# Optimization experiments

Measured on AMD Instinct MI355X. Metric: run time of the kernel, lower is better.

Reference implementation:

```python
import jax, jax.numpy as jnp
import numpy as np

V, E, H = 50000, 100, 128
B, S = 16, 4096
NUM_LEVELS = int(np.log2(S)) + 1  # 13; level l has S >> l nodes
# gate order in the 5-gate stack: i, f_l, f_r, o, u
XMAP = jnp.array([0, 1, 1, 2, 3])


def setup_inputs() -> dict:
    key = jax.random.key(0)
    ks = jax.random.split(key, 9)
    sE = 1.0 / np.sqrt(E)
    sH = 1.0 / np.sqrt(H)
    return {
        "embedding": jax.random.normal(ks[0], (V, E), jnp.float32) * 0.1,
        "W_x": jax.random.normal(ks[1], (4, H, E), jnp.float32) * sE,   # (i,f,o,u) x-projections
        "b_x": jax.random.normal(ks[2], (4, H), jnp.float32) * sE,
        "U_l": jax.random.normal(ks[3], (5, H, H), jnp.float32) * sH,   # (u_i_l,u_f_ll,u_f_rr,u_o_l,u_u_l) applied to h_left
        "b_l": jax.random.normal(ks[4], (5, H), jnp.float32) * sH,
        "U_r": jax.random.normal(ks[5], (5, H, H), jnp.float32) * sH,   # (u_i_r,u_f_lr,u_f_rl,u_o_r,u_u_r) applied to h_right
        "b_r": jax.random.normal(ks[6], (5, H), jnp.float32) * sH,
        "input_seq": jax.random.randint(ks[7], (B, S), 0, V, jnp.int32),
        "dep_tags": jax.random.randint(ks[8], (NUM_LEVELS - 1, S // 2), 0, S, jnp.int32),
    }


def _level_step(x5, h_l, h_r, c_l, c_r, U_l, b_l, U_r, b_r):
    # x5: [B,N,5,H] per-gate x contributions (w_*(x) incl. bias)
    pre = (x5
           + jnp.einsum('bnk,ghk->bngh', h_l, U_l) + b_l
           + jnp.einsum('bnk,ghk->bngh', h_r, U_r) + b_r)  # [B,N,5,H]
    i   = jax.nn.sigmoid(pre[:, :, 0])
    f_l = jax.nn.sigmoid(pre[:, :, 1])
    f_r = jax.nn.sigmoid(pre[:, :, 2])
    o   = jax.nn.sigmoid(pre[:, :, 3])
    u   = jnp.tanh(pre[:, :, 4])
    c = i * u + f_l * c_l + f_r * c_r
    h = o * jnp.tanh(c)
    return h, c


def reference(embedding, W_x, b_x, U_l, b_l, U_r, b_r, input_seq, dep_tags):
    b, s = input_seq.shape
    emb = embedding[input_seq]  # [B,S,E]
    xg = jnp.einsum('bse,ghe->bsgh', emb, W_x) + b_x  # [B,S,4,H]

    # level 0: every leaf is a token, children are zero
    z = jnp.zeros((b, s, xg.shape[-1]), xg.dtype)
    h, c = _level_step(xg[:, :, XMAP, :], z, z, z, z, U_l, b_l, U_r, b_r)

    for l in range(1, NUM_LEVELS):
        n = s >> l
        dep = dep_tags[l - 1, :n]                # token position re-embedded at each internal node
        x5 = xg[:, dep][:, :, XMAP, :]           # [B,N,5,H]
        hp = h.reshape(b, n, 2, -1)              # node i's children are (2i, 2i+1)
        cp = c.reshape(b, n, 2, -1)
        h, c = _level_step(x5, hp[:, :, 0], hp[:, :, 1], cp[:, :, 0], cp[:, :, 1],
                           U_l, b_l, U_r, b_r)
    return h[:, 0], c[:, 0]  # root (h, c): [B,H] each
```

## Files before the change

kernel.cpp:

```cpp
#include <hip/hip_runtime.h>
#include <hip/hip_bf16.h>

#define V_ 50000
#define E_ 100
#define H_ 128
#define B_ 16
#define S_ 4096

typedef unsigned short u16;
typedef unsigned int   u32;
typedef short bf16x8 __attribute__((ext_vector_type(8)));
typedef float f32x4  __attribute__((ext_vector_type(4)));

__device__ __forceinline__ float bf2f(u16 x) {
  return __uint_as_float(((u32)x) << 16);
}
__device__ __forceinline__ u16 f2bf(float x) {
  __hip_bfloat16 b = __float2bfloat16(x);
  return *reinterpret_cast<u16*>(&b);
}
__device__ __forceinline__ float sigm(float x) { return 1.0f / (1.0f + __expf(-x)); }
__device__ __forceinline__ float tanh_f(float x) {
  float e = __expf(2.0f * x);
  return 1.0f - 2.0f / (e + 1.0f);
}

#define PREP_N0 (V_ * 128)
#define PREP_N1 65536
#define PREP_N2 163840
#define PREP_N3 640
__global__ __launch_bounds__(256) void prep_all(
    const float* __restrict__ emb, const float* __restrict__ Wx,
    const float* __restrict__ Ul, const float* __restrict__ Ur,
    const float* __restrict__ bl, const float* __restrict__ br,
    const float* __restrict__ bx,
    u16* __restrict__ embB, u16* __restrict__ Bx, u16* __restrict__ Bu,
    float* __restrict__ bxs, float* __restrict__ bd)
{
  int i = blockIdx.x * 256 + threadIdx.x;
  if (i < PREP_N0) {
    int k = i & 127, t = i >> 7;
    embB[i] = (k < E_) ? f2bf(emb[t * E_ + k]) : (u16)0;
    return;
  }
  i -= PREP_N0;
  if (i < PREP_N1) {
    int j = i & 7, l = (i >> 3) & 63, s = (i >> 9) & 3, t = i >> 11;
    int k = s * 32 + (l >> 4) * 8 + j;
    int o = t * 16 + (l & 15);
    Bx[i] = (k < E_) ? f2bf(Wx[o * E_ + k]) : (u16)0;
    return;
  }
  i -= PREP_N1;
  if (i < PREP_N2) {
    int j = i & 7, l = (i >> 3) & 63, s = (i >> 9) & 7, t = i >> 12;
    int k = s * 32 + (l >> 4) * 8 + j;
    int gh = t * 16 + (l & 15);
    float v = (k < 128) ? Ul[gh * 128 + k] : Ur[gh * 128 + (k - 128)];
    Bu[i] = f2bf(v);
    return;
  }
  i -= PREP_N2;
  if (i < 512) {
    int g = i >> 7, hh = i & 127;
    int lg = (g == 0) ? 0 : (g == 1) ? 1 : (g == 2) ? 3 : 4;
    bxs[i] = bx[i] + bl[lg * 128 + hh] + br[lg * 128 + hh];
    return;
  }
  i -= 512;
  if (i < 128) bd[i] = (bl[256 + i] + br[256 + i]) - (bl[128 + i] + br[128 + i]);
}

#define XLDS 514
__global__ __launch_bounds__(512) void xg_mfma(
    const u16* __restrict__ embB, const u16* __restrict__ Bx,
    const float* __restrict__ bxs, const int* __restrict__ seq,
    ushort4* __restrict__ xg, u16* __restrict__ h0)
{
  __shared__ u16 lds[32 * XLDS];
  const int w = threadIdx.x >> 6, lane = threadIdx.x & 63;
  const int quad = lane >> 4, l15 = lane & 15;
  const int m0 = blockIdx.x * 32;

  f32x4 acc[2][4];
  #pragma unroll
  for (int r = 0; r < 2; ++r)
    #pragma unroll
    for (int t = 0; t < 4; ++t) acc[r][t] = (f32x4){0.f, 0.f, 0.f, 0.f};

  int tok0 = seq[m0 + l15];
  int tok1 = seq[m0 + 16 + l15];
  const u16* a0p = embB + (size_t)tok0 * 128 + quad * 8;
  const u16* a1p = embB + (size_t)tok1 * 128 + quad * 8;

  #pragma unroll
  for (int s = 0; s < 4; ++s) {
    bf16x8 a0 = *reinterpret_cast<const bf16x8*>(a0p + s * 32);
    bf16x8 a1 = *reinterpret_cast<const bf16x8*>(a1p + s * 32);
    #pragma unroll
    for (int ti = 0; ti < 4; ++ti) {
      int t = w * 4 + ti;
      bf16x8 b = *reinterpret_cast<const bf16x8*>(Bx + ((size_t)(t * 4 + s) * 64 + lane) * 8);
      acc[0][ti] = __builtin_amdgcn_mfma_f32_16x16x32_bf16(a0, b, acc[0][ti], 0, 0, 0);
      acc[1][ti] = __builtin_amdgcn_mfma_f32_16x16x32_bf16(a1, b, acc[1][ti], 0, 0, 0);
    }
  }

  const int g = w >> 1;
  #pragma unroll
  for (int ti = 0; ti < 4; ++ti) {
    int o = (w * 4 + ti) * 16 + l15;
    float bxo = bxs[o];
    int hhw = (w & 1) * 64 + ti * 16 + l15;
    #pragma unroll
    for (int r = 0; r < 2; ++r)
      #pragma unroll
      for (int reg = 0; reg < 4; ++reg) {
        int mrow = r * 16 + quad * 4 + reg;
        lds[mrow * XLDS + hhw * 4 + g] = f2bf(acc[r][ti][reg] + bxo);
      }
  }
  __syncthreads();

  #pragma unroll
  for (int i = 0; i < 8; ++i) {
    int pidx = i * 512 + threadIdx.x;
    int m = pidx >> 7, hh = pidx & 127;
    ushort4 v = *reinterpret_cast<const ushort4*>(&lds[m * XLDS + hh * 4]);
    size_t gm = (size_t)(m0 + m);
    xg[gm * 128 + hh] = v;
    float c = sigm(bf2f(v.x)) * tanh_f(bf2f(v.w));
    float h = sigm(bf2f(v.z)) * tanh_f(c);
    h0[gm * 128 + hh] = f2bf(h);
  }
}

template<bool REC>
__global__ __launch_bounds__(512) void level_mfma64(
    const ushort4* __restrict__ xg4, const int* __restrict__ deprow,
    const u16* __restrict__ Bu, const float* __restrict__ bd,
    const u16* __restrict__ hPrev, const float* __restrict__ cPrev,
    u16* __restrict__ hOut, float* __restrict__ cOut, int n, int ln2n)
{
  const int w = threadIdx.x >> 6, lane = threadIdx.x & 63;
  const int quad = lane >> 4, l15 = lane & 15;
  const int hh = w * 16 + l15;
  const int m0 = blockIdx.x * 64;

  ushort4 xv[16];
  #pragma unroll
  for (int i = 0; i < 16; ++i) {
    int m = m0 + (i >> 2) * 16 + quad * 4 + (i & 3);
    int j = m & (n - 1);
    int b = m >> ln2n;
    xv[i] = xg4[((size_t)b * S_ + deprow[j]) * 128 + hh];
  }

  f32x4 acc[4][5];
  #pragma unroll
  for (int r = 0; r < 4; ++r)
    #pragma unroll
    for (int g = 0; g < 5; ++g) acc[r][g] = (f32x4){0.f, 0.f, 0.f, 0.f};

  const u16* ap = hPrev + (size_t)(m0 + l15) * 256 + quad * 8;

  #pragma unroll
  for (int s = 0; s < 8; ++s) {
    bf16x8 a[4];
    #pragma unroll
    for (int r = 0; r < 4; ++r)
      a[r] = *reinterpret_cast<const bf16x8*>(ap + (size_t)r * 16 * 256 + s * 32);
    #pragma unroll
    for (int g = 0; g < 5; ++g) {
      int t = g * 8 + w;
      bf16x8 b = *reinterpret_cast<const bf16x8*>(Bu + ((size_t)(t * 8 + s) * 64 + lane) * 8);
      #pragma unroll
      for (int r = 0; r < 4; ++r)
        acc[r][g] = __builtin_amdgcn_mfma_f32_16x16x32_bf16(a[r], b, acc[r][g], 0, 0, 0);
    }
  }

  float bdv = bd[hh];
  #pragma unroll
  for (int i = 0; i < 16; ++i) {
    int r = i >> 2, reg = i & 3;
    int m = m0 + r * 16 + quad * 4 + reg;
    ushort4 v = xv[i];
    float x0 = bf2f(v.x), x1 = bf2f(v.y), x2 = bf2f(v.z), x3 = bf2f(v.w);
    float cl, cr;
    if constexpr (REC) {
      ushort4 vl = xg4[(size_t)(2 * m) * 128 + hh];
      ushort4 vr = xg4[(size_t)(2 * m + 1) * 128 + hh];
      cl = sigm(bf2f(vl.x)) * tanh_f(bf2f(vl.w));
      cr = sigm(bf2f(vr.x)) * tanh_f(bf2f(vr.w));
    } else {
      cl = cPrev[(size_t)m * 256 + hh];
      cr = cPrev[(size_t)m * 256 + 128 + hh];
    }
    float pi  = acc[r][0][reg] + x0;
    float pfl = acc[r][1][reg] + x1;
    float pfr = acc[r][2][reg] + x1 + bdv;
    float po  = acc[r][3][reg] + x2;
    float pu  = acc[r][4][reg] + x3;
    float c = sigm(pi) * tanh_f(pu) + sigm(pfl) * cl + sigm(pfr) * cr;
    float h = sigm(po) * tanh_f(c);
    hOut[(size_t)m * 128 + hh] = f2bf(h);
    cOut[(size_t)m * 128 + hh] = c;
  }
}

__global__ __launch_bounds__(512) void level_mfma(
    const ushort4* __restrict__ xg4, const int* __restrict__ deprow,
    const u16* __restrict__ Bu, const float* __restrict__ bd,
    const u16* __restrict__ hPrev, const float* __restrict__ cPrev,
    u16* __restrict__ hOut, float* __restrict__ cOut, int n, int ln2n)
{
  const int w = threadIdx.x >> 6, lane = threadIdx.x & 63;
  const int quad = lane >> 4, l15 = lane & 15;
  const int hh = w * 16 + l15;
  const int m0 = blockIdx.x * 32;

  ushort4 xv[8];
  float clv[8], crv[8];
  #pragma unroll
  for (int i = 0; i < 8; ++i) {
    int m = m0 + (i >> 2) * 16 + quad * 4 + (i & 3);
    int j = m & (n - 1);
    int b = m >> ln2n;
    int dj = deprow[j];
    xv[i] = xg4[((size_t)b * S_ + dj) * 128 + hh];
    clv[i] = cPrev[(size_t)m * 256 + hh];
    crv[i] = cPrev[(size_t)m * 256 + 128 + hh];
  }

  f32x4 acc[2][5];
  #pragma unroll
  for (int r = 0; r < 2; ++r)
    #pragma unroll
    for (int g = 0; g < 5; ++g) acc[r][g] = (f32x4){0.f, 0.f, 0.f, 0.f};

  const u16* a0p = hPrev + (size_t)(m0 + l15) * 256 + quad * 8;
  const u16* a1p = a0p + 16 * 256;

  #pragma unroll
  for (int s = 0; s < 8; ++s) {
    bf16x8 a0 = *reinterpret_cast<const bf16x8*>(a0p + s * 32);
    bf16x8 a1 = *reinterpret_cast<const bf16x8*>(a1p + s * 32);
    #pragma unroll
    for (int g = 0; g < 5; ++g) {
      int t = g * 8 + w;
      bf16x8 b = *reinterpret_cast<const bf16x8*>(Bu + ((size_t)(t * 8 + s) * 64 + lane) * 8);
      acc[0][g] = __builtin_amdgcn_mfma_f32_16x16x32_bf16(a0, b, acc[0][g], 0, 0, 0);
      acc[1][g] = __builtin_amdgcn_mfma_f32_16x16x32_bf16(a1, b, acc[1][g], 0, 0, 0);
    }
  }

  float bdv = bd[hh];
  #pragma unroll
  for (int i = 0; i < 8; ++i) {
    int r = i >> 2, reg = i & 3;
    int m = m0 + r * 16 + quad * 4 + reg;
    ushort4 v = xv[i];
    float x0 = bf2f(v.x), x1 = bf2f(v.y), x2 = bf2f(v.z), x3 = bf2f(v.w);
    float pi  = acc[r][0][reg] + x0;
    float pfl = acc[r][1][reg] + x1;
    float pfr = acc[r][2][reg] + x1 + bdv;
    float po  = acc[r][3][reg] + x2;
    float pu  = acc[r][4][reg] + x3;
    float c = sigm(pi) * tanh_f(pu) + sigm(pfl) * clv[i] + sigm(pfr) * crv[i];
    float h = sigm(po) * tanh_f(c);
    hOut[(size_t)m * 128 + hh] = f2bf(h);
    cOut[(size_t)m * 128 + hh] = c;
  }
}

__global__ __launch_bounds__(512) void deep_fused(
    const ushort4* __restrict__ xg4, const int* __restrict__ dep,
    const u16* __restrict__ Bu, const float* __restrict__ bd,
    const u16* __restrict__ h6, const float* __restrict__ c6,
    float* __restrict__ out)
{
  __shared__ u16  hls[2][32 * 136];
  __shared__ float cls[2][32 * 128];
  const int b = blockIdx.x;
  const int w = threadIdx.x >> 6, lane = threadIdx.x & 63;
  const int quad = lane >> 4, l15 = lane & 15;
  const int hh = w * 16 + l15;

  const float bdv = bd[hh];

  {
    ushort4 xv[2][4];
    float clv[2][4], crv[2][4];
    #pragma unroll
    for (int r = 0; r < 2; ++r)
      #pragma unroll
      for (int reg = 0; reg < 4; ++reg) {
        int j = r * 16 + quad * 4 + reg;
        int dj = dep[6 * 2048 + j];
        xv[r][reg] = xg4[((size_t)b * S_ + dj) * 128 + hh];
        clv[r][reg] = c6[(size_t)(b * 32 + j) * 256 + hh];
        crv[r][reg] = c6[(size_t)(b * 32 + j) * 256 + 128 + hh];
      }

    f32x4 acc[2][5];
    #pragma unroll
    for (int r = 0; r < 2; ++r)
      #pragma unroll
      for (int g = 0; g < 5; ++g) acc[r][g] = (f32x4){0.f, 0.f, 0.f, 0.f};

    #pragma unroll
    for (int s = 0; s < 8; ++s) {
      const u16* ap = h6 + (size_t)(b * 32 + l15) * 256 + s * 32 + quad * 8;
      bf16x8 a0 = *reinterpret_cast<const bf16x8*>(ap);
      bf16x8 a1 = *reinterpret_cast<const bf16x8*>(ap + 16 * 256);
      #pragma unroll
      for (int g = 0; g < 5; ++g) {
        int t = g * 8 + w;
        bf16x8 bb = *reinterpret_cast<const bf16x8*>(Bu + ((size_t)(t * 8 + s) * 64 + lane) * 8);
        acc[0][g] = __builtin_amdgcn_mfma_f32_16x16x32_bf16(a0, bb, acc[0][g], 0, 0, 0);
        acc[1][g] = __builtin_amdgcn_mfma_f32_16x16x32_bf16(a1, bb, acc[1][g], 0, 0, 0);
      }
    }

    #pragma unroll
    for (int r = 0; r < 2; ++r)
      #pragma unroll
      for (int reg = 0; reg < 4; ++reg) {
        int j = r * 16 + quad * 4 + reg;
        ushort4 v = xv[r][reg];
        float x0 = bf2f(v.x), x1 = bf2f(v.y), x2 = bf2f(v.z), x3 = bf2f(v.w);
        float pi  = acc[r][0][reg] + x0;
        float pfl = acc[r][1][reg] + x1;
        float pfr = acc[r][2][reg] + x1 + bdv;
        float po  = acc[r][3][reg] + x2;
        float pu  = acc[r][4][reg] + x3;
        float c = sigm(pi) * tanh_f(pu) + sigm(pfl) * clv[r][reg] + sigm(pfr) * crv[r][reg];
        float h = sigm(po) * tanh_f(c);
        hls[0][j * 136 + hh] = f2bf(h);
        cls[0][j * 128 + hh] = c;
      }
  }
  __syncthreads();

  ushort4 xvc[4];
  #pragma unroll
  for (int reg = 0; reg < 4; ++reg)
    xvc[reg] = xg4[((size_t)b * S_ + dep[7 * 2048 + quad * 4 + reg]) * 128 + hh];

  int pb = 0;
  for (int lvl = 8; lvl <= 12; ++lvl) {
    int nb = 4096 >> lvl;

    ushort4 xvn[4];
    if (lvl < 12) {
      int nbn = 2048 >> lvl;
      #pragma unroll
      for (int reg = 0; reg < 4; ++reg) {
        int j = quad * 4 + reg;
        if (j < nbn)
          xvn[reg] = xg4[((size_t)b * S_ + dep[lvl * 2048 + j]) * 128 + hh];
      }
    }

    f32x4 acc[5];
    #pragma unroll
    for (int g = 0; g < 5; ++g) acc[g] = (f32x4){0.f, 0.f, 0.f, 0.f};

    #pragma unroll
    for (int s = 0; s < 8; ++s) {
      int child = 2 * l15 + (s >= 4 ? 1 : 0);
      int kk = (s & 3) * 32 + quad * 8;
      bf16x8 a = *reinterpret_cast<const bf16x8*>(&hls[pb][child * 136 + kk]);
      #pragma unroll
      for (int g = 0; g < 5; ++g) {
        int t = g * 8 + w;
        bf16x8 bb = *reinterpret_cast<const bf16x8*>(Bu + ((size_t)(t * 8 + s) * 64 + lane) * 8);
        acc[g] = __builtin_amdgcn_mfma_f32_16x16x32_bf16(a, bb, acc[g], 0, 0, 0);
      }
    }

    #pragma unroll
    for (int reg = 0; reg < 4; ++reg) {
      int j = quad * 4 + reg;
      if (j < nb) {
        ushort4 v = xvc[reg];
        float x0 = bf2f(v.x), x1 = bf2f(v.y), x2 = bf2f(v.z), x3 = bf2f(v.w);
        float cl = cls[pb][(2 * j) * 128 + hh];
        float cr = cls[pb][(2 * j + 1) * 128 + hh];
        float pi  = acc[0][reg] + x0;
        float pfl = acc[1][reg] + x1;
        float pfr = acc[2][reg] + x1 + bdv;
        float po  = acc[3][reg] + x2;
        float pu  = acc[4][reg] + x3;
        float c = sigm(pi) * tanh_f(pu) + sigm(pfl) * cl + sigm(pfr) * cr;
        float h = sigm(po) * tanh_f(c);
        hls[pb ^ 1][j * 136 + hh] = f2bf(h);
        cls[pb ^ 1][j * 128 + hh] = c;
        if (lvl == 12) {
          out[b * 128 + hh] = h;
          out[2048 + b * 128 + hh] = c;
        }
      }
    }
    __syncthreads();
    pb ^= 1;
    #pragma unroll
    for (int reg = 0; reg < 4; ++reg) xvc[reg] = xvn[reg];
  }
}

extern "C" void kernel_launch(void* const* d_in, const int* in_sizes, int n_in,
                              void* d_out, int out_size, void* d_ws, size_t ws_size,
                              hipStream_t stream)
{
  const float* emb = (const float*)d_in[0];
  const float* Wx  = (const float*)d_in[1];
  const float* bx  = (const float*)d_in[2];
  const float* Ul  = (const float*)d_in[3];
  const float* bl  = (const float*)d_in[4];
  const float* Ur  = (const float*)d_in[5];
  const float* br  = (const float*)d_in[6];
  const int* seq = (const int*)d_in[7];
  const int* dep = (const int*)d_in[8];

  char* p = (char*)d_ws;
  u16* embB = (u16*)p;    p += (size_t)V_ * 128 * 2;
  u16* BswX = (u16*)p;    p += 131072;
  u16* BswU = (u16*)p;    p += 327680;
  float* bxs = (float*)p; p += 2048;
  float* bd = (float*)p;  p += 2048;
  u16* xg = (u16*)p;      p += (size_t)B_ * S_ * 512 * 2;
  u16* h0 = (u16*)p;      p += (size_t)B_ * S_ * 128 * 2;
  u16* hA = (u16*)p;      p += (size_t)32768 * 128 * 2;
  float* cA = (float*)p;  p += (size_t)32768 * 128 * 4;
  u16* hB = (u16*)p;      p += (size_t)16384 * 128 * 2;
  float* cB = (float*)p;  p += (size_t)16384 * 128 * 4;

  const int prep_tot = PREP_N0 + PREP_N1 + PREP_N2 + PREP_N3;
  prep_all<<<dim3((prep_tot + 255) / 256), dim3(256), 0, stream>>>(
      emb, Wx, Ul, Ur, bl, br, bx, embB, BswX, BswU, bxs, bd);

  xg_mfma<<<dim3(B_ * S_ / 32), dim3(512), 0, stream>>>(
      embB, BswX, bxs, seq, (ushort4*)xg, h0);

  const ushort4* xg4 = (const ushort4*)xg;

  level_mfma64<true><<<dim3(32768 / 64), dim3(512), 0, stream>>>(
      xg4, dep, BswU, bd, h0, (const float*)nullptr, hA, cA, 2048, 11);

  u16 *hp = hA, *ho = hB;
  float *cp = cA, *co = cB;
  for (int l = 2; l <= 3; ++l) {
    int n = S_ >> l;
    int Mtot = B_ * n;
    const int* deprow = dep + (size_t)(l - 1) * (S_ / 2);
    level_mfma64<false><<<dim3(Mtot / 64), dim3(512), 0, stream>>>(
        xg4, deprow, BswU, bd, hp, cp, ho, co, n, 12 - l);
    u16* th = hp; hp = ho; ho = th;
    float* tc = cp; cp = co; co = tc;
  }
  for (int l = 4; l <= 6; ++l) {
    int n = S_ >> l;
    int Mtot = B_ * n;
    const int* deprow = dep + (size_t)(l - 1) * (S_ / 2);
    level_mfma<<<dim3(Mtot / 32), dim3(512), 0, stream>>>(
        xg4, deprow, BswU, bd, hp, cp, ho, co, n, 12 - l);
    u16* th = hp; hp = ho; ho = th;
    float* tc = cp; cp = co; co = tc;
  }

  deep_fused<<<dim3(16), dim3(512), 0, stream>>>(
      xg4, dep, BswU, bd, hp, cp, (float*)d_out);
}
```

Measured before the change: 276.7 us.

## Fuse tree levels pairwise in LDS and store leaf cell state

Replaces the per-level launches for levels 1-6 with a level_pair kernel that computes two consecutive tree levels per block. The intermediate h/c stay in shared memory, so every other level's global write and read disappear and launches drop from six to three. The leaf kernel now writes c0 to global memory instead of having level 1 recompute it from xg. In exchange, the later launches are small (128 and 32 blocks), which lowers occupancy, and the extra c0 write adds memory traffic.

```diff
diff --git a/kernel.cpp b/kernel.cpp
--- a/kernel.cpp
+++ b/kernel.cpp
@@ -75,7 +75,7 @@
 __global__ __launch_bounds__(512) void xg_mfma(
     const u16* __restrict__ embB, const u16* __restrict__ Bx,
     const float* __restrict__ bxs, const int* __restrict__ seq,
-    ushort4* __restrict__ xg, u16* __restrict__ h0)
+    ushort4* __restrict__ xg, u16* __restrict__ h0, float* __restrict__ c0)
 {
   __shared__ u16 lds[32 * XLDS];
   const int w = threadIdx.x >> 6, lane = threadIdx.x & 63;
@@ -132,20 +132,34 @@
     float c = sigm(bf2f(v.x)) * tanh_f(bf2f(v.w));
     float h = sigm(bf2f(v.z)) * tanh_f(c);
     h0[gm * 128 + hh] = f2bf(h);
-  }
-}
-
-template<bool REC>
-__global__ __launch_bounds__(512) void level_mfma64(
-    const ushort4* __restrict__ xg4, const int* __restrict__ deprow,
+    c0[gm * 128 + hh] = c;
+  }
+}
+
+__global__ __launch_bounds__(512) void level_pair(
+    const ushort4* __restrict__ xg4,
+    const int* __restrict__ deprow1, const int* __restrict__ deprow2,
     const u16* __restrict__ Bu, const float* __restrict__ bd,
     const u16* __restrict__ hPrev, const float* __restrict__ cPrev,
-    u16* __restrict__ hOut, float* __restrict__ cOut, int n, int ln2n)
+    u16* __restrict__ hOut2, float* __restrict__ cOut2, int n, int ln2n)
 {
+  __shared__ u16  hls[64 * 136];
+  __shared__ float cls[64 * 128];
   const int w = threadIdx.x >> 6, lane = threadIdx.x & 63;
   const int quad = lane >> 4, l15 = lane & 15;
   const int hh = w * 16 + l15;
   const int m0 = blockIdx.x * 64;
+  const int M02 = blockIdx.x * 32;
+  const int n2 = n >> 1;
+
+  int row2[8];
+  #pragma unroll
+  for (int i = 0; i < 8; ++i) {
+    int m2 = M02 + (i >> 2) * 16 + quad * 4 + (i & 3);
+    int j2 = m2 & (n2 - 1);
+    int b2 = m2 >> (ln2n - 1);
+    row2[i] = b2 * S_ + deprow2[j2];
+  }
 
   ushort4 xv[16];
   #pragma unroll
@@ -153,7 +167,7 @@
     int m = m0 + (i >> 2) * 16 + quad * 4 + (i & 3);
     int j = m & (n - 1);
     int b = m >> ln2n;
-    xv[i] = xg4[((size_t)b * S_ + deprow[j]) * 128 + hh];
+    xv[i] = xg4[((size_t)b * S_ + deprow1[j]) * 128 + hh];
   }
 
   f32x4 acc[4][5];
@@ -180,23 +194,22 @@
     }
   }
 
+  ushort4 xv2[8];
+  #pragma unroll
+  for (int i = 0; i < 8; ++i)
+    xv2[i] = xg4[(size_t)row2[i] * 128 + hh];
+
   float bdv = bd[hh];
+
   #pragma unroll
   for (int i = 0; i < 16; ++i) {
     int r = i >> 2, reg = i & 3;
     int m = m0 + r * 16 + quad * 4 + reg;
+    int lr = m - m0;
     ushort4 v = xv[i];
     float x0 = bf2f(v.x), x1 = bf2f(v.y), x2 = bf2f(v.z), x3 = bf2f(v.w);
-    float cl, cr;
-    if constexpr (REC) {
-      ushort4 vl = xg4[(size_t)(2 * m) * 128 + hh];
-      ushort4 vr = xg4[(size_t)(2 * m + 1) * 128 + hh];
-      cl = sigm(bf2f(vl.x)) * tanh_f(bf2f(vl.w));
-      cr = sigm(bf2f(vr.x)) * tanh_f(bf2f(vr.w));
-    } else {
-      cl = cPrev[(size_t)m * 256 + hh];
-      cr = cPrev[(size_t)m * 256 + 128 + hh];
-    }
+    float cl = cPrev[(size_t)m * 256 + hh];
+    float cr = cPrev[(size_t)m * 256 + 128 + hh];
     float pi  = acc[r][0][reg] + x0;
     float pfl = acc[r][1][reg] + x1;
     float pfr = acc[r][2][reg] + x1 + bdv;
@@ -204,73 +217,50 @@
     float pu  = acc[r][4][reg] + x3;
     float c = sigm(pi) * tanh_f(pu) + sigm(pfl) * cl + sigm(pfr) * cr;
     float h = sigm(po) * tanh_f(c);
-    hOut[(size_t)m * 128 + hh] = f2bf(h);
-    cOut[(size_t)m * 128 + hh] = c;
-  }
-}
-
-__global__ __launch_bounds__(512) void level_mfma(
-    const ushort4* __restrict__ xg4, const int* __restrict__ deprow,
-    const u16* __restrict__ Bu, const float* __restrict__ bd,
-    const u16* __restrict__ hPrev, const float* __restrict__ cPrev,
-    u16* __restrict__ hOut, float* __restrict__ cOut, int n, int ln2n)
-{
-  const int w = threadIdx.x >> 6, lane = threadIdx.x & 63;
-  const int quad = lane >> 4, l15 = lane & 15;
-  const int hh = w * 16 + l15;
-  const int m0 = blockIdx.x * 32;
-
-  ushort4 xv[8];
-  float clv[8], crv[8];
-  #pragma unroll
-  for (int i = 0; i < 8; ++i) {
-    int m = m0 + (i >> 2) * 16 + quad * 4 + (i & 3);
-    int j = m & (n - 1);
-    int b = m >> ln2n;
-    int dj = deprow[j];
-    xv[i] = xg4[((size_t)b * S_ + dj) * 128 + hh];
-    clv[i] = cPrev[(size_t)m * 256 + hh];
-    crv[i] = cPrev[(size_t)m * 256 + 128 + hh];
-  }
-
-  f32x4 acc[2][5];
+    hls[lr * 136 + hh] = f2bf(h);
+    cls[lr * 128 + hh] = c;
+  }
+  __syncthreads();
+
+  f32x4 acc2[2][5];
   #pragma unroll
   for (int r = 0; r < 2; ++r)
     #pragma unroll
-    for (int g = 0; g < 5; ++g) acc[r][g] = (f32x4){0.f, 0.f, 0.f, 0.f};
-
-  const u16* a0p = hPrev + (size_t)(m0 + l15) * 256 + quad * 8;
-  const u16* a1p = a0p + 16 * 256;
+    for (int g = 0; g < 5; ++g) acc2[r][g] = (f32x4){0.f, 0.f, 0.f, 0.f};
 
   #pragma unroll
   for (int s = 0; s < 8; ++s) {
-    bf16x8 a0 = *reinterpret_cast<const bf16x8*>(a0p + s * 32);
-    bf16x8 a1 = *reinterpret_cast<const bf16x8*>(a1p + s * 32);
+    int child = 2 * l15 + (s >= 4 ? 1 : 0);
+    int kk = (s & 3) * 32 + quad * 8;
+    bf16x8 a0 = *reinterpret_cast<const bf16x8*>(&hls[child * 136 + kk]);
+    bf16x8 a1 = *reinterpret_cast<const bf16x8*>(&hls[(child + 32) * 136 + kk]);
     #pragma unroll
     for (int g = 0; g < 5; ++g) {
       int t = g * 8 + w;
-      bf16x8 b = *reinterpret_cast<const bf16x8*>(Bu + ((size_t)(t * 8 + s) * 64 + lane) * 8);
-      acc[0][g] = __builtin_amdgcn_mfma_f32_16x16x32_bf16(a0, b, acc[0][g], 0, 0, 0);
-      acc[1][g] = __builtin_amdgcn_mfma_f32_16x16x32_bf16(a1, b, acc[1][g], 0, 0, 0);
-    }
-  }
-
-  float bdv = bd[hh];
+      bf16x8 bb = *reinterpret_cast<const bf16x8*>(Bu + ((size_t)(t * 8 + s) * 64 + lane) * 8);
+      acc2[0][g] = __builtin_amdgcn_mfma_f32_16x16x32_bf16(a0, bb, acc2[0][g], 0, 0, 0);
+      acc2[1][g] = __builtin_amdgcn_mfma_f32_16x16x32_bf16(a1, bb, acc2[1][g], 0, 0, 0);
+    }
+  }
+
   #pragma unroll
   for (int i = 0; i < 8; ++i) {
     int r = i >> 2, reg = i & 3;
-    int m = m0 + r * 16 + quad * 4 + reg;
-    ushort4 v = xv[i];
+    int m2 = M02 + r * 16 + quad * 4 + reg;
+    int lj = r * 16 + quad * 4 + reg;
+    ushort4 v = xv2[i];
     float x0 = bf2f(v.x), x1 = bf2f(v.y), x2 = bf2f(v.z), x3 = bf2f(v.w);
-    float pi  = acc[r][0][reg] + x0;
-    float pfl = acc[r][1][reg] + x1;
-    float pfr = acc[r][2][reg] + x1 + bdv;
-    float po  = acc[r][3][reg] + x2;
-    float pu  = acc[r][4][reg] + x3;
-    float c = sigm(pi) * tanh_f(pu) + sigm(pfl) * clv[i] + sigm(pfr) * crv[i];
+    float cl = cls[(2 * lj) * 128 + hh];
+    float cr = cls[(2 * lj + 1) * 128 + hh];
+    float pi  = acc2[r][0][reg] + x0;
+    float pfl = acc2[r][1][reg] + x1;
+    float pfr = acc2[r][2][reg] + x1 + bdv;
+    float po  = acc2[r][3][reg] + x2;
+    float pu  = acc2[r][4][reg] + x3;
+    float c = sigm(pi) * tanh_f(pu) + sigm(pfl) * cl + sigm(pfr) * cr;
     float h = sigm(po) * tanh_f(c);
-    hOut[(size_t)m * 128 + hh] = f2bf(h);
-    cOut[(size_t)m * 128 + hh] = c;
+    hOut2[(size_t)m2 * 128 + hh] = f2bf(h);
+    cOut2[(size_t)m2 * 128 + hh] = c;
   }
 }
 
@@ -432,44 +422,30 @@
   float* bd = (float*)p;  p += 2048;
   u16* xg = (u16*)p;      p += (size_t)B_ * S_ * 512 * 2;
   u16* h0 = (u16*)p;      p += (size_t)B_ * S_ * 128 * 2;
-  u16* hA = (u16*)p;      p += (size_t)32768 * 128 * 2;
-  float* cA = (float*)p;  p += (size_t)32768 * 128 * 4;
-  u16* hB = (u16*)p;      p += (size_t)16384 * 128 * 2;
-  float* cB = (float*)p;  p += (size_t)16384 * 128 * 4;
+  float* c0 = (float*)p;  p += (size_t)B_ * S_ * 128 * 4;
+  u16* hL2 = (u16*)p;     p += (size_t)16384 * 128 * 2;
+  float* cL2 = (float*)p; p += (size_t)16384 * 128 * 4;
+  u16* hL4 = (u16*)p;     p += (size_t)4096 * 128 * 2;
+  float* cL4 = (float*)p; p += (size_t)4096 * 128 * 4;
+  u16* hL6 = (u16*)p;     p += (size_t)1024 * 128 * 2;
+  float* cL6 = (float*)p; p += (size_t)1024 * 128 * 4;
 
   const int prep_tot = PREP_N0 + PREP_N1 + PREP_N2 + PREP_N3;
   prep_all<<<dim3((prep_tot + 255) / 256), dim3(256), 0, stream>>>(
       emb, Wx, Ul, Ur, bl, br, bx, embB, BswX, BswU, bxs, bd);
 
   xg_mfma<<<dim3(B_ * S_ / 32), dim3(512), 0, stream>>>(
-      embB, BswX, bxs, seq, (ushort4*)xg, h0);
+      embB, BswX, bxs, seq, (ushort4*)xg, h0, c0);
 
   const ushort4* xg4 = (const ushort4*)xg;
 
-  level_mfma64<true><<<dim3(32768 / 64), dim3(512), 0, stream>>>(
-      xg4, dep, BswU, bd, h0, (const float*)nullptr, hA, cA, 2048, 11);
-
-  u16 *hp = hA, *ho = hB;
-  float *cp = cA, *co = cB;
-  for (int l = 2; l <= 3; ++l) {
-    int n = S_ >> l;
-    int Mtot = B_ * n;
-    const int* deprow = dep + (size_t)(l - 1) * (S_ / 2);
-    level_mfma64<false><<<dim3(Mtot / 64), dim3(512), 0, stream>>>(
-        xg4, deprow, BswU, bd, hp, cp, ho, co, n, 12 - l);
-    u16* th = hp; hp = ho; ho = th;
-    float* tc = cp; cp = co; co = tc;
-  }
-  for (int l = 4; l <= 6; ++l) {
-    int n = S_ >> l;
-    int Mtot = B_ * n;
-    const int* deprow = dep + (size_t)(l - 1) * (S_ / 2);
-    level_mfma<<<dim3(Mtot / 32), dim3(512), 0, stream>>>(
-        xg4, deprow, BswU, bd, hp, cp, ho, co, n, 12 - l);
-    u16* th = hp; hp = ho; ho = th;
-    float* tc = cp; cp = co; co = tc;
-  }
+  level_pair<<<dim3(512), dim3(512), 0, stream>>>(
+      xg4, dep, dep + 2048, BswU, bd, h0, c0, hL2, cL2, 2048, 11);
+  level_pair<<<dim3(128), dim3(512), 0, stream>>>(
+      xg4, dep + 2 * 2048, dep + 3 * 2048, BswU, bd, hL2, cL2, hL4, cL4, 512, 9);
+  level_pair<<<dim3(32), dim3(512), 0, stream>>>(
+      xg4, dep + 4 * 2048, dep + 5 * 2048, BswU, bd, hL4, cL4, hL6, cL6, 128, 7);
 
   deep_fused<<<dim3(16), dim3(512), 0, stream>>>(
-      xg4, dep, BswU, bd, hp, cp, (float*)d_out);
-}
+      xg4, dep, BswU, bd, hL6, cL6, (float*)d_out);
+}
```

Result: slower. 282.5 us (+2.1%).
